# Performance work log

Hardware: AMD Instinct MI355X
Metric: run time of the kernel (lower is better)

Reference implementation:

```python
import jax, jax.numpy as jnp
import numpy as np

LN_EPS = 1e-5

def _layernorm(x, g, b):
    mu = jnp.mean(x, axis=-1, keepdims=True)
    var = jnp.var(x, axis=-1, keepdims=True)
    return (x - mu) / jnp.sqrt(var + LN_EPS) * g + b

def setup_inputs() -> dict:
    key = jax.random.key(0)
    ks = jax.random.split(key, 12)
    N, D_WSI, D_OMIC, D, DH = 50000, 1024, 1577, 256, 128
    def rn(k, shape, s=0.02):
        return jax.random.normal(k, shape, jnp.float32) * s
    return {
        'wsi': jax.random.normal(ks[0], (N, D_WSI), jnp.float32),
        'x_omic': jax.random.normal(ks[1], (D_OMIC,), jnp.float32),
        # SNNOmics: Linear(1577,256)+ELU, Linear(256,256)+ELU (AlphaDropout=eval identity)
        'W1': rn(ks[2], (D_OMIC, 256)), 'b1': jnp.zeros((256,), jnp.float32),
        'W2': rn(ks[3], (256, 256)), 'b2': jnp.zeros((256,), jnp.float32),
        # wsi projection Linear(1024,256)
        'Wp': rn(ks[4], (D_WSI, D)), 'bp': jnp.zeros((D,), jnp.float32),
        # MMAttentionLayer pre-norm (dim=256)
        'ln1_g': jnp.ones((D,), jnp.float32), 'ln1_b': jnp.zeros((D,), jnp.float32),
        # to_qkv: Linear(256, 3*heads*dim_head) = Linear(256, 384), no bias (heads=1, dim_head=128)
        'Wqkv': rn(ks[5], (D, 3 * DH)),
        # FeedForward(dim=128, mult=1): LN + Linear(128,128)+GELU+Linear(128,128) (no residual)
        'ln2_g': jnp.ones((DH,), jnp.float32), 'ln2_b': jnp.zeros((DH,), jnp.float32),
        'Wf1': rn(ks[6], (DH, DH)), 'bf1': jnp.zeros((DH,), jnp.float32),
        'Wf2': rn(ks[7], (DH, DH)), 'bf2': jnp.zeros((DH,), jnp.float32),
        # final LayerNorm(128)
        'ln3_g': jnp.ones((DH,), jnp.float32), 'ln3_b': jnp.zeros((DH,), jnp.float32),
        # to_logits: Linear(256,64)+ReLU+Linear(64,4)
        'Wl1': rn(ks[8], (2 * DH, 64)), 'bl1': jnp.zeros((64,), jnp.float32),
        'Wl2': rn(ks[9], (64, 4)), 'bl2': jnp.zeros((4,), jnp.float32),
    }

def reference(wsi, x_omic, W1, b1, W2, b2, Wp, bp, ln1_g, ln1_b, Wqkv,
              ln2_g, ln2_b, Wf1, bf1, Wf2, bf2, ln3_g, ln3_b, Wl1, bl1, Wl2, bl2):
    M = 1            # num_pathways
    DH = 128         # dim_head (heads=1)
    scale = DH ** -0.5
    # SNN omics encoder -> one pathway token [1, 256]
    h = jax.nn.elu(x_omic @ W1 + b1)
    h = jax.nn.elu(h @ W2 + b2)
    h_omic = h[None, :]                              # [1, 256]
    # WSI projection -> histology tokens [N, 256]
    wsi_embed = wsi @ Wp + bp                        # [N, 256]
    tokens = jnp.concatenate([h_omic, wsi_embed], axis=0)   # [1+N, 256]
    # MMAttentionLayer: pre-norm then asymmetric pathway/histology attention
    xn = _layernorm(tokens, ln1_g, ln1_b)
    qkv = xn @ Wqkv                                  # [1+N, 384]
    q, k, v = jnp.split(qkv, 3, axis=-1)             # each [1+N, 128]
    q = q * scale
    q_p, q_h = q[:M], q[M:]                          # [1,128], [N,128]
    k_p, k_h = k[:M], k[M:]
    # cross attention: histology -> pathways (rows of length M=1)
    cross_attn_hist = q_h @ k_p.T                    # [N, 1]
    cross_attn_hist = jax.nn.softmax(cross_attn_hist, axis=-1)
    # pathway row attends to [pathways | histology]
    attn_p = q_p @ k_p.T                             # [1, 1]
    cross_attn_p = q_p @ k_h.T                       # [1, N]
    attn_ph = jax.nn.softmax(jnp.concatenate([attn_p, cross_attn_p], axis=-1), axis=-1)  # [1, 1+N]
    out_p = attn_ph @ v                              # [1, 128]
    out_h = cross_attn_hist @ v[:M]                  # [N, 128]
    out = jnp.concatenate([out_p, out_h], axis=0)    # [1+N, 128] (residual=False: no conv)
    # FeedForward (no residual add in original) + LayerNorm
    mm = _layernorm(out, ln2_g, ln2_b)
    mm = jax.nn.gelu(mm @ Wf1 + bf1, approximate=False) @ Wf2 + bf2
    mm = _layernorm(mm, ln3_g, ln3_b)                # [1+N, 128]
    paths_embed = jnp.mean(mm[:M], axis=0)           # [128]
    wsi_embed_post = jnp.mean(mm[M:], axis=0)        # [128]
    embedding = jnp.concatenate([paths_embed, wsi_embed_post])[None, :]  # [1, 256]
    logits = jax.nn.relu(embedding @ Wl1 + bl1) @ Wl2 + bl2              # [1, 4]
    prob = jax.nn.softmax(logits, axis=-1)
    return logits, prob
```

## Files before the change

kernel.cpp:

```cpp
#include <hip/hip_runtime.h>
#include <hip/hip_bf16.h>
#include <math.h>

#define LN_EPS 1e-5f

typedef unsigned short ushortT;
typedef short bf16x8 __attribute__((ext_vector_type(8)));
typedef float f32x4 __attribute__((ext_vector_type(4)));

#define WS_QP   0
#define WS_V0   128
#define WS_S0   256
#define WS_H1P  512
#define WS_PART 4608
#define PART_STRIDE 132
#define PART_M 128
#define PART_L 129
#define WS_GP   109000
#define GP_STRIDE 132
#define NCOMB   32
#define WS_WPT  131072
#define WS_WKVT 262144

__device__ __forceinline__ float elu1(float x){ return x > 0.f ? x : expm1f(x); }
__device__ __forceinline__ unsigned pk2(float lo, float hi){
  union { __hip_bfloat162 h; unsigned u; } cv;
  cv.h = __float22bfloat162_rn(make_float2(lo, hi));
  return cv.u;
}
__device__ __forceinline__ void dma16(const void* g, void* l) {
  __builtin_amdgcn_global_load_lds(
      (const __attribute__((address_space(1))) unsigned int*)g,
      (__attribute__((address_space(3))) unsigned int*)l, 16, 0, 0);
}
template<int N> __device__ __forceinline__ void vwait() {
  asm volatile("s_waitcnt vmcnt(%0)" :: "i"(N) : "memory");
}
__device__ __forceinline__ void lwait0() {
  asm volatile("s_waitcnt lgkmcnt(0)" ::: "memory");
}
__device__ __forceinline__ void sbar()   { __builtin_amdgcn_s_barrier(); }
__device__ __forceinline__ void schedb() { __builtin_amdgcn_sched_barrier(0); }

__global__ __launch_bounds__(256) void k_setup(
    const float* __restrict__ Wp, const float* __restrict__ Wqkv,
    const float* __restrict__ x, const float* __restrict__ W1, int d_omic,
    ushortT* __restrict__ wpt, ushortT* __restrict__ wkvt, float* __restrict__ ws)
{
  int bb = blockIdx.x, t = threadIdx.x;
  if (bb < 32) {
    int kc = bb, m = t, sw = (m >> 1) & 3;
    #pragma unroll
    for (int c = 0; c < 4; ++c) {
      float v[8];
      #pragma unroll
      for (int e = 0; e < 8; ++e) v[e] = Wp[(size_t)(kc * 32 + c * 8 + e) * 256 + m];
      uint4 w = make_uint4(pk2(v[0], v[1]), pk2(v[2], v[3]), pk2(v[4], v[5]), pk2(v[6], v[7]));
      *(uint4*)&wpt[kc * 8192 + m * 32 + ((c ^ sw) * 8)] = w;
    }
  } else if (bb < 40) {
    int kk = bb - 32, m = t, sw = (m >> 1) & 3;
    #pragma unroll
    for (int c = 0; c < 4; ++c) {
      float v[8];
      #pragma unroll
      for (int e = 0; e < 8; ++e) v[e] = Wqkv[(size_t)(kk * 32 + c * 8 + e) * 384 + 128 + m];
      uint4 w = make_uint4(pk2(v[0], v[1]), pk2(v[2], v[3]), pk2(v[4], v[5]), pk2(v[6], v[7]));
      *(uint4*)&wkvt[kk * 8192 + m * 32 + ((c ^ sw) * 8)] = w;
    }
  } else {
    int g = bb - 40;
    int i0 = g * 99, i1 = min(i0 + 99, d_omic);
    __shared__ float xs[112];
    for (int i = i0 + t; i < i1; i += 256) xs[i - i0] = x[i];
    __syncthreads();
    float s = 0.f;
    for (int i = i0; i < i1; i++) s = fmaf(xs[i - i0], W1[(size_t)i * 256 + t], s);
    ws[WS_H1P + g * 256 + t] = s;
  }
}

__global__ __launch_bounds__(256) void k_omic(
    const float* __restrict__ b1,
    const float* __restrict__ W2, const float* __restrict__ b2,
    const float* __restrict__ Wqkv,
    const float* __restrict__ ln1_g, const float* __restrict__ ln1_b,
    float* __restrict__ ws)
{
  __shared__ float h1[256];
  __shared__ float xn0[256];
  __shared__ float qs[128], ks[128];
  __shared__ float red[8];
  int tid = threadIdx.x, lane = tid & 63, wave = tid >> 6;

  float s = b1[tid];
  for (int g = 0; g < 16; g++) s += ws[WS_H1P + g * 256 + tid];
  h1[tid] = elu1(s);
  __syncthreads();

  s = b2[tid];
  for (int i = 0; i < 256; i++) s = fmaf(h1[i], W2[i * 256 + tid], s);
  float t0 = elu1(s);

  float ps = t0, pq = t0 * t0;
  for (int m = 1; m < 64; m <<= 1) { ps += __shfl_xor(ps, m); pq += __shfl_xor(pq, m); }
  if (lane == 0) { red[wave] = ps; red[4 + wave] = pq; }
  __syncthreads();
  float mu = (red[0] + red[1] + red[2] + red[3]) * (1.f / 256.f);
  float var = (red[4] + red[5] + red[6] + red[7]) * (1.f / 256.f) - mu * mu;
  float xn = (t0 - mu) * rsqrtf(var + LN_EPS) * ln1_g[tid] + ln1_b[tid];
  xn0[tid] = xn;
  __syncthreads();

  float a = 0.f;
  for (int j = 0; j < 256; j++) a = fmaf(xn0[j], Wqkv[j * 384 + tid], a);
  if (tid < 128) { float q = a * 0.088388347648318447f; qs[tid] = q; ws[WS_QP + tid] = q; }
  else           { ks[tid - 128] = a; }
  if (tid < 128) {
    float av = 0.f;
    for (int j = 0; j < 256; j++) av = fmaf(xn0[j], Wqkv[j * 384 + 256 + tid], av);
    ws[WS_V0 + tid] = av;
  }
  __syncthreads();
  float p = (tid < 128) ? qs[tid] * ks[tid] : 0.f;
  for (int m = 1; m < 64; m <<= 1) p += __shfl_xor(p, m);
  if (lane == 0) red[wave] = p;
  __syncthreads();
  if (tid == 0) ws[WS_S0] = red[0] + red[1] + red[2] + red[3];
}

__global__ __launch_bounds__(1024, 4) void k_main(
    const float* __restrict__ wsi, int N,
    const ushortT* __restrict__ wpt, const ushortT* __restrict__ wkvt,
    const float* __restrict__ bp,
    const float* __restrict__ ln1_g, const float* __restrict__ ln1_b,
    float* __restrict__ ws)
{
  __shared__ __align__(16) char U[131072];

  const int tid = threadIdx.x;
  const int lane = tid & 63, wv = tid >> 6;
  const int l15 = lane & 15, lh = lane >> 4;
  const int cg = wv & 3, rg = wv >> 2;
  const int b = blockIdx.x, r0 = b * 256;

  int wsiSrc[2];
  #pragma unroll
  for (int i = 0; i < 2; ++i) {
    int rowL = 16 * wv + 8 * i + (lane >> 3);
    int gr = r0 + rowL; gr = (gr < N) ? gr : (N - 1);
    wsiSrc[i] = gr * 1024 + (((lane & 7) ^ (lane >> 3)) << 2);
  }
  const int wptSrc = (16 * wv) * 32 + lane * 8;

  const unsigned afslot = (unsigned)((lh ^ ((l15 >> 1) & 3)) << 4);
  const unsigned bs0 = (unsigned)(((2 * lh)     ^ (l15 & 7)) << 4);
  const unsigned bs1 = (unsigned)(((2 * lh + 1) ^ (l15 & 7)) << 4);

  const f32x4 z4 = {0.f, 0.f, 0.f, 0.f};
  f32x4 acc[4][4];
  #pragma unroll
  for (int mt = 0; mt < 4; ++mt)
    #pragma unroll
    for (int nt = 0; nt < 4; ++nt) acc[mt][nt] = z4;

  auto dmaSlice = [&](int kc, int k) {
    char* ds = U + k * 32768 + wv * 2048;
    #pragma unroll
    for (int i = 0; i < 2; ++i) dma16(wsi + wsiSrc[i] + kc * 32, ds + i * 1024);
    char* dw = U + 65536 + k * 16384 + wv * 1024;
    dma16(wpt + wptSrc + kc * 8192, dw);
  };

  dmaSlice(0, 0);
  for (int s = 0; s < 32; ++s) {
    if (s < 31) { dmaSlice(s + 1, (s + 1) & 1); vwait<3>(); }
    else vwait<0>();
    sbar(); schedb();
    {
      const char* Ws = U + (s & 1) * 32768;
      const char* Wf = U + 65536 + (s & 1) * 16384;
      bf16x8 af[4], bfr[4];
      #pragma unroll
      for (int mt = 0; mt < 4; ++mt)
        af[mt] = *(const bf16x8*)(Wf + (64 * cg + 16 * mt + l15) * 64 + afslot);
      #pragma unroll
      for (int nt = 0; nt < 4; ++nt) {
        const char* p = Ws + (64 * rg + 16 * nt + l15) * 128;
        uint4 ua = *(const uint4*)(p + bs0);
        uint4 ub = *(const uint4*)(p + bs1);
        union { unsigned u[4]; bf16x8 v; } cv;
        cv.u[0] = pk2(__uint_as_float(ua.x), __uint_as_float(ua.y));
        cv.u[1] = pk2(__uint_as_float(ua.z), __uint_as_float(ua.w));
        cv.u[2] = pk2(__uint_as_float(ub.x), __uint_as_float(ub.y));
        cv.u[3] = pk2(__uint_as_float(ub.z), __uint_as_float(ub.w));
        bfr[nt] = cv.v;
      }
      #pragma unroll
      for (int mt = 0; mt < 4; ++mt)
        #pragma unroll
        for (int nt = 0; nt < 4; ++nt)
          acc[mt][nt] = __builtin_amdgcn_mfma_f32_16x16x32_bf16(af[mt], bfr[nt], acc[mt][nt], 0, 0, 0);
    }
    sbar(); schedb();
  }

  float* red = (float*)(U + 98304);
  float4 bp4[4], g4[4], b4[4];
  #pragma unroll
  for (int mt = 0; mt < 4; ++mt) {
    int m0 = 64 * cg + 16 * mt + 4 * lh;
    bp4[mt] = *(const float4*)&bp[m0];
    g4[mt]  = *(const float4*)&ln1_g[m0];
    b4[mt]  = *(const float4*)&ln1_b[m0];
  }
  float ps[4], pq[4];
  #pragma unroll
  for (int nt = 0; nt < 4; ++nt) { ps[nt] = 0.f; pq[nt] = 0.f; }
  #pragma unroll
  for (int mt = 0; mt < 4; ++mt) {
    const float bb4[4] = {bp4[mt].x, bp4[mt].y, bp4[mt].z, bp4[mt].w};
    #pragma unroll
    for (int nt = 0; nt < 4; ++nt)
      #pragma unroll
      for (int r = 0; r < 4; ++r) {
        float v = acc[mt][nt][r] + bb4[r];
        acc[mt][nt][r] = v;
        ps[nt] += v; pq[nt] += v * v;
      }
  }
  #pragma unroll
  for (int nt = 0; nt < 4; ++nt) {
    ps[nt] += __shfl_xor(ps[nt], 16); pq[nt] += __shfl_xor(pq[nt], 16);
    ps[nt] += __shfl_xor(ps[nt], 32); pq[nt] += __shfl_xor(pq[nt], 32);
  }
  if (lh == 0) {
    #pragma unroll
    for (int nt = 0; nt < 4; ++nt) {
      int row = 64 * rg + 16 * nt + l15;
      *(float2*)&red[row * 8 + cg * 2] = make_float2(ps[nt], pq[nt]);
    }
  }
  lwait0(); sbar(); schedb();
  float mu[4], rstd[4];
  #pragma unroll
  for (int nt = 0; nt < 4; ++nt) {
    int row = 64 * rg + 16 * nt + l15;
    float s_ = 0.f, q_ = 0.f;
    #pragma unroll
    for (int c = 0; c < 4; ++c) { s_ += red[row * 8 + c * 2]; q_ += red[row * 8 + c * 2 + 1]; }
    float m_ = s_ * (1.f / 256.f);
    float v_ = q_ * (1.f / 256.f) - m_ * m_;
    mu[nt] = m_; rstd[nt] = rsqrtf(v_ + LN_EPS);
  }
  lwait0(); sbar(); schedb();

  #pragma unroll
  for (int nt = 0; nt < 4; ++nt) {
    int row = 64 * rg + 16 * nt + l15;
    unsigned rswz = (unsigned)((row & 7) << 4);
    #pragma unroll
    for (int mt = 0; mt < 4; ++mt) {
      float x0 = (acc[mt][nt][0] - mu[nt]) * rstd[nt] * g4[mt].x + b4[mt].x;
      float x1 = (acc[mt][nt][1] - mu[nt]) * rstd[nt] * g4[mt].y + b4[mt].y;
      float x2 = (acc[mt][nt][2] - mu[nt]) * rstd[nt] * g4[mt].z + b4[mt].z;
      float x3 = (acc[mt][nt][3] - mu[nt]) * rstd[nt] * g4[mt].w + b4[mt].w;
      unsigned off = (unsigned)(row * 512 + (64 * cg + 16 * mt + 4 * lh) * 2) ^ rswz;
      *(uint2*)(U + off) = make_uint2(pk2(x0, x1), pk2(x2, x3));
    }
  }
  lwait0(); sbar(); schedb();

  f32x4 acc2[4][4];
  #pragma unroll
  for (int mt = 0; mt < 4; ++mt)
    #pragma unroll
    for (int nt = 0; nt < 4; ++nt) acc2[mt][nt] = z4;
  int kvBase[4];
  #pragma unroll
  for (int mt = 0; mt < 4; ++mt) {
    int m = 64 * cg + 16 * mt + l15;
    kvBase[mt] = m * 32 + ((lh ^ ((m >> 1) & 3)) << 3);
  }
  bf16x8 gA[4], gB[4];
  #pragma unroll
  for (int mt = 0; mt < 4; ++mt) gA[mt] = *(const bf16x8*)(wkvt + kvBase[mt]);
  #pragma unroll
  for (int kp = 0; kp < 4; ++kp) {
    const int kk0 = 2 * kp, kk1 = 2 * kp + 1;
    #pragma unroll
    for (int mt = 0; mt < 4; ++mt)
      gB[mt] = *(const bf16x8*)(wkvt + kvBase[mt] + kk1 * 8192);
    {
      bf16x8 bfr[4];
      #pragma unroll
      for (int nt = 0; nt < 4; ++nt) {
        int row = 64 * rg + 16 * nt + l15;
        unsigned off = (unsigned)(row * 512 + kk0 * 64 + lh * 16) ^ (unsigned)((row & 7) << 4);
        bfr[nt] = *(const bf16x8*)(U + off);
      }
      #pragma unroll
      for (int mt = 0; mt < 4; ++mt)
        #pragma unroll
        for (int nt = 0; nt < 4; ++nt)
          acc2[mt][nt] = __builtin_amdgcn_mfma_f32_16x16x32_bf16(gA[mt], bfr[nt], acc2[mt][nt], 0, 0, 0);
    }
    if (kp < 3) {
      #pragma unroll
      for (int mt = 0; mt < 4; ++mt)
        gA[mt] = *(const bf16x8*)(wkvt + kvBase[mt] + (kk0 + 2) * 8192);
    }
    {
      bf16x8 bfr[4];
      #pragma unroll
      for (int nt = 0; nt < 4; ++nt) {
        int row = 64 * rg + 16 * nt + l15;
        unsigned off = (unsigned)(row * 512 + kk1 * 64 + lh * 16) ^ (unsigned)((row & 7) << 4);
        bfr[nt] = *(const bf16x8*)(U + off);
      }
      #pragma unroll
      for (int mt = 0; mt < 4; ++mt)
        #pragma unroll
        for (int nt = 0; nt < 4; ++nt)
          acc2[mt][nt] = __builtin_amdgcn_mfma_f32_16x16x32_bf16(gB[mt], bfr[nt], acc2[mt][nt], 0, 0, 0);
    }
  }
  sbar(); schedb();

  float* sred = (float*)U;
  float* aux  = (float*)(U + 2048);
  float* wts  = (float*)(U + 2112);
  float* vred = (float*)(U + 3200);
  float* part = ws + WS_PART + (size_t)b * PART_STRIDE;

  if (cg < 2) {
    float4 qp4[4];
    #pragma unroll
    for (int mt = 0; mt < 4; ++mt)
      qp4[mt] = *(const float4*)&ws[WS_QP + 64 * cg + 16 * mt + 4 * lh];
    float sp[4];
    #pragma unroll
    for (int nt = 0; nt < 4; ++nt) {
      float s_ = 0.f;
      #pragma unroll
      for (int mt = 0; mt < 4; ++mt) {
        s_ = fmaf(qp4[mt].x, acc2[mt][nt][0], s_);
        s_ = fmaf(qp4[mt].y, acc2[mt][nt][1], s_);
        s_ = fmaf(qp4[mt].z, acc2[mt][nt][2], s_);
        s_ = fmaf(qp4[mt].w, acc2[mt][nt][3], s_);
      }
      sp[nt] = s_;
    }
    #pragma unroll
    for (int nt = 0; nt < 4; ++nt) {
      sp[nt] += __shfl_xor(sp[nt], 16);
      sp[nt] += __shfl_xor(sp[nt], 32);
    }
    if (lh == 0) {
      #pragma unroll
      for (int nt = 0; nt < 4; ++nt) sred[cg * 256 + 64 * rg + 16 * nt + l15] = sp[nt];
    }
  }
  lwait0(); sbar(); schedb();

  float sv = -INFINITY, ev = 0.f;
  if (tid < 256) {
    sv = sred[tid] + sred[256 + tid];
    if (r0 + tid >= N) sv = -INFINITY;
  }
  float mb = sv;
  #pragma unroll
  for (int m = 1; m < 64; m <<= 1) mb = fmaxf(mb, __shfl_xor(mb, m));
  if (tid < 256 && lane == 0) aux[tid >> 6] = mb;
  lwait0(); sbar(); schedb();
  float M2 = fmaxf(fmaxf(aux[0], aux[1]), fmaxf(aux[2], aux[3]));
  if (tid < 256) { ev = (r0 + tid < N) ? expf(sv - M2) : 0.f; wts[tid] = ev; }
  float lsum = ev;
  #pragma unroll
  for (int m = 1; m < 64; m <<= 1) lsum += __shfl_xor(lsum, m);
  if (tid < 256 && lane == 0) aux[4 + (tid >> 6)] = lsum;
  lwait0(); sbar(); schedb();
  if (tid == 0) { part[PART_M] = M2; part[PART_L] = aux[4] + aux[5] + aux[6] + aux[7]; }

  if (cg >= 2) {
    float wr[4];
    #pragma unroll
    for (int nt = 0; nt < 4; ++nt) wr[nt] = wts[64 * rg + 16 * nt + l15];
    #pragma unroll
    for (int mt = 0; mt < 4; ++mt) {
      float vs0 = 0.f, vs1 = 0.f, vs2 = 0.f, vs3 = 0.f;
      #pragma unroll
      for (int nt = 0; nt < 4; ++nt) {
        vs0 = fmaf(wr[nt], acc2[mt][nt][0], vs0);
        vs1 = fmaf(wr[nt], acc2[mt][nt][1], vs1);
        vs2 = fmaf(wr[nt], acc2[mt][nt][2], vs2);
        vs3 = fmaf(wr[nt], acc2[mt][nt][3], vs3);
      }
      #pragma unroll
      for (int m = 1; m < 16; m <<= 1) {
        vs0 += __shfl_xor(vs0, m); vs1 += __shfl_xor(vs1, m);
        vs2 += __shfl_xor(vs2, m); vs3 += __shfl_xor(vs3, m);
      }
      if (l15 == 0)
        *(float4*)&vred[128 * rg + 64 * (cg - 2) + 16 * mt + 4 * lh] =
            make_float4(vs0, vs1, vs2, vs3);
    }
  }
  lwait0(); sbar(); schedb();
  if (tid < 128)
    part[tid] = vred[tid] + vred[128 + tid] + vred[256 + tid] + vred[384 + tid];
}

__global__ __launch_bounds__(128) void k_fin1(float* __restrict__ ws, int NB, int chunk)
{
  int g = blockIdx.x, col = threadIdx.x;
  int c0 = g * chunk, c1 = min(c0 + chunk, NB);
  const float* part = ws + WS_PART;
  float mg = -INFINITY;
  for (int bb = c0; bb < c1; ++bb)
    mg = fmaxf(mg, part[(size_t)bb * PART_STRIDE + PART_M]);
  float a = 0.f, lg = 0.f;
  for (int bb = c0; bb < c1; ++bb) {
    float w = expf(part[(size_t)bb * PART_STRIDE + PART_M] - mg);
    a  = fmaf(part[(size_t)bb * PART_STRIDE + col], w, a);
    lg = fmaf(part[(size_t)bb * PART_STRIDE + PART_L], w, lg);
  }
  ws[WS_GP + g * GP_STRIDE + col] = a;
  if (col == 0) {
    ws[WS_GP + g * GP_STRIDE + 128] = mg;
    ws[WS_GP + g * GP_STRIDE + 129] = lg;
  }
}

__global__ __launch_bounds__(256) void k_final(
    const float* __restrict__ ws,
    const float* __restrict__ Wf1, const float* __restrict__ bf1,
    const float* __restrict__ Wf2, const float* __restrict__ bf2,
    const float* __restrict__ ln2_g, const float* __restrict__ ln2_b,
    const float* __restrict__ ln3_g, const float* __restrict__ ln3_b,
    const float* __restrict__ Wl1, const float* __restrict__ bl1,
    const float* __restrict__ Wl2, const float* __restrict__ bl2,
    float* __restrict__ out)
{
  __shared__ float rowb[2][128];
  __shared__ float mmb[2][128];
  __shared__ float red[8];
  __shared__ float emb[256];
  __shared__ float abuf[64];
  __shared__ float lbuf[4];
  __shared__ float wg[NCOMB];
  __shared__ float MLs[2];
  int tid = threadIdx.x, lane = tid & 63, wave = tid >> 6;
  float s0 = ws[WS_S0];

  if (tid == 0) {
    float M = s0;
    for (int g = 0; g < NCOMB; ++g) M = fmaxf(M, ws[WS_GP + g * GP_STRIDE + 128]);
    float L = expf(s0 - M);
    for (int g = 0; g < NCOMB; ++g)
      L = fmaf(ws[WS_GP + g * GP_STRIDE + 129], expf(ws[WS_GP + g * GP_STRIDE + 128] - M), L);
    MLs[0] = M; MLs[1] = L;
  }
  __syncthreads();
  float M = MLs[0], L = MLs[1];
  if (tid < NCOMB) wg[tid] = expf(ws[WS_GP + tid * GP_STRIDE + 128] - M);
  __syncthreads();

  if (tid < 128) {
    float v0 = ws[WS_V0 + tid];
    float a = v0 * expf(s0 - M);
    #pragma unroll
    for (int g = 0; g < NCOMB; ++g) a = fmaf(ws[WS_GP + g * GP_STRIDE + tid], wg[g], a);
    rowb[0][tid] = a / L;
    rowb[1][tid] = v0;
  }
  __syncthreads();

  int row = tid >> 7, k = tid & 127;
  float x = rowb[row][k];
  float ps = x, pq = x * x;
  for (int m = 1; m < 64; m <<= 1) { ps += __shfl_xor(ps, m); pq += __shfl_xor(pq, m); }
  __syncthreads();
  if (lane == 0) { red[wave] = ps; red[4 + wave] = pq; }
  __syncthreads();
  {
    float sum = red[row * 2] + red[row * 2 + 1];
    float sq  = red[4 + row * 2] + red[4 + row * 2 + 1];
    float mu = sum * (1.f / 128.f);
    float var = sq * (1.f / 128.f) - mu * mu;
    x = (x - mu) * rsqrtf(var + LN_EPS) * ln2_g[k] + ln2_b[k];
  }
  mmb[row][k] = x;
  __syncthreads();
  float t1 = bf1[k];
  for (int j = 0; j < 128; j++) t1 = fmaf(mmb[row][j], Wf1[j * 128 + k], t1);
  float gg = t1 * 0.5f * (1.f + erff(t1 * 0.70710678118654752f));
  __syncthreads();
  rowb[row][k] = gg;
  __syncthreads();
  float t2 = bf2[k];
  for (int j = 0; j < 128; j++) t2 = fmaf(rowb[row][j], Wf2[j * 128 + k], t2);
  ps = t2; pq = t2 * t2;
  for (int m = 1; m < 64; m <<= 1) { ps += __shfl_xor(ps, m); pq += __shfl_xor(pq, m); }
  __syncthreads();
  if (lane == 0) { red[wave] = ps; red[4 + wave] = pq; }
  __syncthreads();
  {
    float sum = red[row * 2] + red[row * 2 + 1];
    float sq  = red[4 + row * 2] + red[4 + row * 2 + 1];
    float mu = sum * (1.f / 128.f);
    float var = sq * (1.f / 128.f) - mu * mu;
    t2 = (t2 - mu) * rsqrtf(var + LN_EPS) * ln3_g[k] + ln3_b[k];
  }
  emb[row * 128 + k] = t2;
  __syncthreads();
  if (tid < 64) {
    float a = bl1[tid];
    for (int j = 0; j < 256; j++) a = fmaf(emb[j], Wl1[j * 64 + tid], a);
    abuf[tid] = fmaxf(a, 0.f);
  }
  __syncthreads();
  if (tid < 4) {
    float lg = bl2[tid];
    for (int j = 0; j < 64; j++) lg = fmaf(abuf[j], Wl2[j * 4 + tid], lg);
    lbuf[tid] = lg;
  }
  __syncthreads();
  if (tid < 4) {
    float m4 = fmaxf(fmaxf(lbuf[0], lbuf[1]), fmaxf(lbuf[2], lbuf[3]));
    float e0 = expf(lbuf[0] - m4), e1 = expf(lbuf[1] - m4);
    float e2 = expf(lbuf[2] - m4), e3 = expf(lbuf[3] - m4);
    float ssum = e0 + e1 + e2 + e3;
    out[tid] = lbuf[tid];
    out[4 + tid] = expf(lbuf[tid] - m4) / ssum;
  }
}

extern "C" void kernel_launch(void* const* d_in, const int* in_sizes, int n_in,
                              void* d_out, int out_size, void* d_ws, size_t ws_size,
                              hipStream_t stream) {
  const float* wsi    = (const float*)d_in[0];
  const float* x_omic = (const float*)d_in[1];
  const float* W1     = (const float*)d_in[2];
  const float* b1     = (const float*)d_in[3];
  const float* W2     = (const float*)d_in[4];
  const float* b2     = (const float*)d_in[5];
  const float* Wp     = (const float*)d_in[6];
  const float* bp     = (const float*)d_in[7];
  const float* ln1_g  = (const float*)d_in[8];
  const float* ln1_b  = (const float*)d_in[9];
  const float* Wqkv   = (const float*)d_in[10];
  const float* ln2_g  = (const float*)d_in[11];
  const float* ln2_b  = (const float*)d_in[12];
  const float* Wf1    = (const float*)d_in[13];
  const float* bf1    = (const float*)d_in[14];
  const float* Wf2    = (const float*)d_in[15];
  const float* bf2    = (const float*)d_in[16];
  const float* ln3_g  = (const float*)d_in[17];
  const float* ln3_b  = (const float*)d_in[18];
  const float* Wl1    = (const float*)d_in[19];
  const float* bl1    = (const float*)d_in[20];
  const float* Wl2    = (const float*)d_in[21];
  const float* bl2    = (const float*)d_in[22];
  float* ws   = (float*)d_ws;
  float* outp = (float*)d_out;
  ushortT* wpt  = (ushortT*)(ws + WS_WPT);
  ushortT* wkvt = (ushortT*)(ws + WS_WKVT);

  int N = in_sizes[0] / 1024;
  int d_omic = in_sizes[1];
  int NB = (N + 255) / 256;
  int chunk = (NB + NCOMB - 1) / NCOMB;

  k_setup<<<56, 256, 0, stream>>>(Wp, Wqkv, x_omic, W1, d_omic, wpt, wkvt, ws);
  k_omic<<<1, 256, 0, stream>>>(b1, W2, b2, Wqkv, ln1_g, ln1_b, ws);
  k_main<<<NB, 1024, 0, stream>>>(wsi, N, wpt, wkvt, bp, ln1_g, ln1_b, ws);
  k_fin1<<<NCOMB, 128, 0, stream>>>(ws, NB, chunk);
  k_final<<<1, 256, 0, stream>>>(ws, Wf1, bf1, Wf2, bf2, ln2_g, ln2_b,
                                 ln3_g, ln3_b, Wl1, bl1, Wl2, bl2, outp);
}
```

Before: 141.2 us.

## Halve k_main tile to 128 rows and deepen wsi prefetch to three stages

Shrinks each k_main block from 1024 threads and 256 rows to 512 threads and 128 rows, cutting LDS from 128KB to 80KB so more blocks can be resident per CU. The wsi staging becomes a triple buffer and the Wp slice a double buffer, with loads issued after compute so more slices are in flight. One redundant barrier is dropped. The cost is twice as many blocks, which means more partials for k_fin1 and each block re-reading the full Wp from cache.

```diff
diff --git a/kernel.cpp b/kernel.cpp
--- a/kernel.cpp
+++ b/kernel.cpp
@@ -129,20 +129,20 @@
   if (tid == 0) ws[WS_S0] = red[0] + red[1] + red[2] + red[3];
 }
 
-__global__ __launch_bounds__(1024, 4) void k_main(
+__global__ __launch_bounds__(512, 4) void k_main(
     const float* __restrict__ wsi, int N,
     const ushortT* __restrict__ wpt, const ushortT* __restrict__ wkvt,
     const float* __restrict__ bp,
     const float* __restrict__ ln1_g, const float* __restrict__ ln1_b,
     float* __restrict__ ws)
 {
-  __shared__ __align__(16) char U[131072];
+  __shared__ __align__(16) char U[81920];
 
   const int tid = threadIdx.x;
   const int lane = tid & 63, wv = tid >> 6;
   const int l15 = lane & 15, lh = lane >> 4;
   const int cg = wv & 3, rg = wv >> 2;
-  const int b = blockIdx.x, r0 = b * 256;
+  const int b = blockIdx.x, r0 = b * 128;
 
   int wsiSrc[2];
   #pragma unroll
@@ -151,7 +151,9 @@
     int gr = r0 + rowL; gr = (gr < N) ? gr : (N - 1);
     wsiSrc[i] = gr * 1024 + (((lane & 7) ^ (lane >> 3)) << 2);
   }
-  const int wptSrc = (16 * wv) * 32 + lane * 8;
+  int wptSrc[2];
+  #pragma unroll
+  for (int j = 0; j < 2; ++j) wptSrc[j] = (32 * wv + 16 * j) * 32 + lane * 8;
 
   const unsigned afslot = (unsigned)((lh ^ ((l15 >> 1) & 3)) << 4);
   const unsigned bs0 = (unsigned)(((2 * lh)     ^ (l15 & 7)) << 4);
@@ -164,22 +166,26 @@
     #pragma unroll
     for (int nt = 0; nt < 4; ++nt) acc[mt][nt] = z4;
 
-  auto dmaSlice = [&](int kc, int k) {
-    char* ds = U + k * 32768 + wv * 2048;
+  auto stageWsi = [&](int kc, int slot) {
+    char* ds = U + slot * 16384 + wv * 2048;
     #pragma unroll
     for (int i = 0; i < 2; ++i) dma16(wsi + wsiSrc[i] + kc * 32, ds + i * 1024);
-    char* dw = U + 65536 + k * 16384 + wv * 1024;
-    dma16(wpt + wptSrc + kc * 8192, dw);
   };
-
-  dmaSlice(0, 0);
+  auto stageWpt = [&](int kc, int slot) {
+    char* dw = U + 49152 + slot * 16384 + wv * 2048;
+    #pragma unroll
+    for (int j = 0; j < 2; ++j) dma16(wpt + wptSrc[j] + kc * 8192, dw + j * 1024);
+  };
+
+  stageWsi(0, 0); stageWpt(0, 0);
+  stageWsi(1, 1); stageWpt(1, 1);
+  stageWsi(2, 2);
   for (int s = 0; s < 32; ++s) {
-    if (s < 31) { dmaSlice(s + 1, (s + 1) & 1); vwait<3>(); }
-    else vwait<0>();
+    if (s < 30) vwait<6>(); else if (s == 30) vwait<4>(); else vwait<0>();
     sbar(); schedb();
     {
-      const char* Ws = U + (s & 1) * 32768;
-      const char* Wf = U + 65536 + (s & 1) * 16384;
+      const char* Ws = U + (s % 3) * 16384;
+      const char* Wf = U + 49152 + (s & 1) * 16384;
       bf16x8 af[4], bfr[4];
       #pragma unroll
       for (int mt = 0; mt < 4; ++mt)
@@ -203,9 +209,11 @@
           acc[mt][nt] = __builtin_amdgcn_mfma_f32_16x16x32_bf16(af[mt], bfr[nt], acc[mt][nt], 0, 0, 0);
     }
     sbar(); schedb();
-  }
-
-  float* red = (float*)(U + 98304);
+    if (s < 30) stageWpt(s + 2, s & 1);
+    if (s < 29) stageWsi(s + 3, s % 3);
+  }
+
+  float* red = (float*)(U + 65536);
   float4 bp4[4], g4[4], b4[4];
   #pragma unroll
   for (int mt = 0; mt < 4; ++mt) {
@@ -253,8 +261,6 @@
     float v_ = q_ * (1.f / 256.f) - m_ * m_;
     mu[nt] = m_; rstd[nt] = rsqrtf(v_ + LN_EPS);
   }
-  lwait0(); sbar(); schedb();
-
   #pragma unroll
   for (int nt = 0; nt < 4; ++nt) {
     int row = 64 * rg + 16 * nt + l15;
@@ -328,9 +334,9 @@
   sbar(); schedb();
 
   float* sred = (float*)U;
-  float* aux  = (float*)(U + 2048);
-  float* wts  = (float*)(U + 2112);
-  float* vred = (float*)(U + 3200);
+  float* aux  = (float*)(U + 1024);
+  float* wts  = (float*)(U + 1056);
+  float* vred = (float*)(U + 1600);
   float* part = ws + WS_PART + (size_t)b * PART_STRIDE;
 
   if (cg < 2) {
@@ -358,29 +364,29 @@
     }
     if (lh == 0) {
       #pragma unroll
-      for (int nt = 0; nt < 4; ++nt) sred[cg * 256 + 64 * rg + 16 * nt + l15] = sp[nt];
+      for (int nt = 0; nt < 4; ++nt) sred[cg * 128 + 64 * rg + 16 * nt + l15] = sp[nt];
     }
   }
   lwait0(); sbar(); schedb();
 
   float sv = -INFINITY, ev = 0.f;
-  if (tid < 256) {
-    sv = sred[tid] + sred[256 + tid];
+  if (tid < 128) {
+    sv = sred[tid] + sred[128 + tid];
     if (r0 + tid >= N) sv = -INFINITY;
   }
   float mb = sv;
   #pragma unroll
   for (int m = 1; m < 64; m <<= 1) mb = fmaxf(mb, __shfl_xor(mb, m));
-  if (tid < 256 && lane == 0) aux[tid >> 6] = mb;
+  if (tid < 128 && lane == 0) aux[tid >> 6] = mb;
   lwait0(); sbar(); schedb();
-  float M2 = fmaxf(fmaxf(aux[0], aux[1]), fmaxf(aux[2], aux[3]));
-  if (tid < 256) { ev = (r0 + tid < N) ? expf(sv - M2) : 0.f; wts[tid] = ev; }
+  float M2 = fmaxf(aux[0], aux[1]);
+  if (tid < 128) { ev = (r0 + tid < N) ? expf(sv - M2) : 0.f; wts[tid] = ev; }
   float lsum = ev;
   #pragma unroll
   for (int m = 1; m < 64; m <<= 1) lsum += __shfl_xor(lsum, m);
-  if (tid < 256 && lane == 0) aux[4 + (tid >> 6)] = lsum;
+  if (tid < 128 && lane == 0) aux[2 + (tid >> 6)] = lsum;
   lwait0(); sbar(); schedb();
-  if (tid == 0) { part[PART_M] = M2; part[PART_L] = aux[4] + aux[5] + aux[6] + aux[7]; }
+  if (tid == 0) { part[PART_M] = M2; part[PART_L] = aux[2] + aux[3]; }
 
   if (cg >= 2) {
     float wr[4];
@@ -407,8 +413,7 @@
     }
   }
   lwait0(); sbar(); schedb();
-  if (tid < 128)
-    part[tid] = vred[tid] + vred[128 + tid] + vred[256 + tid] + vred[384 + tid];
+  if (tid < 128) part[tid] = vred[tid] + vred[128 + tid];
 }
 
 __global__ __launch_bounds__(128) void k_fin1(float* __restrict__ ws, int NB, int chunk)
@@ -569,12 +574,12 @@
 
   int N = in_sizes[0] / 1024;
   int d_omic = in_sizes[1];
-  int NB = (N + 255) / 256;
+  int NB = (N + 127) / 128;
   int chunk = (NB + NCOMB - 1) / NCOMB;
 
   k_setup<<<56, 256, 0, stream>>>(Wp, Wqkv, x_omic, W1, d_omic, wpt, wkvt, ws);
   k_omic<<<1, 256, 0, stream>>>(b1, W2, b2, Wqkv, ln1_g, ln1_b, ws);
-  k_main<<<NB, 1024, 0, stream>>>(wsi, N, wpt, wkvt, bp, ln1_g, ln1_b, ws);
+  k_main<<<NB, 512, 0, stream>>>(wsi, N, wpt, wkvt, bp, ln1_g, ln1_b, ws);
   k_fin1<<<NCOMB, 128, 0, stream>>>(ws, NB, chunk);
   k_final<<<1, 256, 0, stream>>>(ws, Wf1, bf1, Wf2, bf2, ln2_g, ln2_b,
                                  ln3_g, ln3_b, Wl1, bl1, Wl2, bl2, outp);
```

Measured after the change: 135.9 us. 1.04x faster.
